# Optimization experiments

Hardware: AMD Instinct MI355X
Metric: run time of the kernel (lower is better)

## Reference

```python
import jax, jax.numpy as jnp
import numpy as np

B, T, F = 4096, 60, 64
H = 128          # num_hidden[0] == num_hidden[1]
FC1_IN, FC1_OUT = T * H, 512   # 7680 -> 512
LEN_OUT = 60


def setup_inputs() -> dict:
    key = jax.random.key(0)
    ks = jax.random.split(key, 14)
    s1 = 1.0 / np.sqrt(H)
    def u(k, shape, s):
        return jax.random.uniform(k, shape, jnp.float32, -s, s)
    return {
        "X_cont": jax.random.normal(ks[0], (B, T, F), jnp.float32),
        # LSTM layer 1 (PyTorch gate order i,f,g,o)
        "W_ih1": u(ks[1], (4 * H, F), s1),
        "W_hh1": u(ks[2], (4 * H, H), s1),
        "b_ih1": u(ks[3], (4 * H,), s1),
        "b_hh1": u(ks[4], (4 * H,), s1),
        # LSTM layer 2
        "W_ih2": u(ks[5], (4 * H, H), s1),
        "W_hh2": u(ks[6], (4 * H, H), s1),
        "b_ih2": u(ks[7], (4 * H,), s1),
        "b_hh2": u(ks[8], (4 * H,), s1),
        # FC head
        "W_fc1": u(ks[9], (FC1_OUT, FC1_IN), 1.0 / np.sqrt(FC1_IN)),
        "b_fc1": u(ks[10], (FC1_OUT,), 1.0 / np.sqrt(FC1_IN)),
        "W_fc2": u(ks[11], (LEN_OUT, FC1_OUT), 1.0 / np.sqrt(FC1_OUT)),
        "b_fc2": u(ks[12], (LEN_OUT,), 1.0 / np.sqrt(FC1_OUT)),
    }


def _lstm_layer(x, W_ih, W_hh, b_ih, b_hh):
    # x: [B,T,Fin]; zero initial (h,c); returns full hidden sequence [B,T,H]
    b, h = x.shape[0], W_hh.shape[1]
    # precompute input contribution for all timesteps (one big GEMM)
    xg = jnp.einsum('btf,gf->btg', x, W_ih) + b_ih + b_hh  # [B,T,4H]

    def step(carry, xt):
        hp, cp = carry
        g = xt + hp @ W_hh.T                                # [B,4H]
        i, f, gg, o = jnp.split(g, 4, axis=-1)
        i = jax.nn.sigmoid(i)
        f = jax.nn.sigmoid(f)
        gg = jnp.tanh(gg)
        o = jax.nn.sigmoid(o)
        c = f * cp + i * gg
        hn = o * jnp.tanh(c)
        return (hn, c), hn

    h0 = jnp.zeros((b, h), x.dtype)
    _, hs = jax.lax.scan(step, (h0, h0), jnp.swapaxes(xg, 0, 1))  # [T,B,H]
    return jnp.swapaxes(hs, 0, 1)


def reference(X_cont, W_ih1, W_hh1, b_ih1, b_hh1,
              W_ih2, W_hh2, b_ih2, b_hh2,
              W_fc1, b_fc1, W_fc2, b_fc2):
    b = X_cont.shape[0]
    h1 = _lstm_layer(X_cont, W_ih1, W_hh1, b_ih1, b_hh1)   # [B,T,H]
    h2 = _lstm_layer(h1, W_ih2, W_hh2, b_ih2, b_hh2)       # [B,T,H]
    flat = h2.reshape(b, -1)                               # [B, T*H] = [B,7680]
    fc1 = flat @ W_fc1.T + b_fc1                           # [B,512]
    fc2 = fc1 @ W_fc2.T + b_fc2                            # [B,length_out]
    return fc2.reshape(b, LEN_OUT, 1)
```

## Files before the change

kernel.cpp:

```cpp
#include <hip/hip_runtime.h>
#include <hip/hip_fp16.h>
#include <cstdint>

typedef _Float16 h16;
typedef _Float16 half8 __attribute__((ext_vector_type(8)));
typedef float floatx4 __attribute__((ext_vector_type(4)));

#define T_SZ 60
#define H_SZ 128
#define NB_FC1 7680
#define NKT   240

#define LOG2E  1.44269504088896340736f
#define LOG2E2 2.88539008177792681472f

__device__ __forceinline__ float sigm(float x) {
    float e = __builtin_amdgcn_exp2f(x * -LOG2E);
    return __builtin_amdgcn_rcpf(1.0f + e);
}
__device__ __forceinline__ float tanh_f(float x) {
    float e = __builtin_amdgcn_exp2f(x * LOG2E2);
    return 1.0f - 2.0f * __builtin_amdgcn_rcpf(e + 1.0f);
}

template<int INDIM, bool IN_F32, bool FUSE_FC>
__global__ __launch_bounds__(512, 1)
void lstm_layer(const void* __restrict__ in_v,
                const float* __restrict__ W_ih,
                const float* __restrict__ W_hh,
                const float* __restrict__ b_ih,
                const float* __restrict__ b_hh,
                h16* __restrict__ h_out,
                const h16* __restrict__ WcT,
                const float* __restrict__ bcv,
                float* __restrict__ out)
{
    constexpr int KT_IN = INDIM / 32;
    __shared__ __align__(16) h16 hist[16][16][H_SZ];

    const int tid  = threadIdx.x;
    const int w    = tid >> 6;
    const int lane = tid & 63;
    const int lrow = lane & 15;
    const int lgrp = lane >> 4;
    const size_t base_row = (size_t)blockIdx.x * 16;

    half8 wf_in[4][KT_IN];
    half8 wf_hh[4][4];
    float bias[4];

    #pragma unroll
    for (int q = 0; q < 4; ++q) {
        const int n = (w + 8 * q) * 16 + lrow;
        bias[q] = b_ih[n] + b_hh[n];
        #pragma unroll
        for (int kt = 0; kt < KT_IN; ++kt) {
            const float* p = W_ih + (size_t)n * INDIM + kt * 32 + lgrp * 8;
            half8 v;
            #pragma unroll
            for (int j = 0; j < 8; ++j) v[j] = (h16)p[j];
            wf_in[q][kt] = v;
        }
        #pragma unroll
        for (int kt = 0; kt < 4; ++kt) {
            const float* p = W_hh + (size_t)n * H_SZ + kt * 32 + lgrp * 8;
            half8 v;
            #pragma unroll
            for (int j = 0; j < 8; ++j) v[j] = (h16)p[j];
            wf_hh[q][kt] = v;
        }
    }

    const float* inF = (const float*)in_v;
    const h16*   inH = (const h16*)in_v;

    floatx4 raw[KT_IN][2];
    half8   xs[KT_IN];

    auto load_x = [&](int t) {
        #pragma unroll
        for (int kt = 0; kt < KT_IN; ++kt) {
            if constexpr (IN_F32) {
                const float* p = inF + ((base_row + lrow) * T_SZ + t) * INDIM + kt * 32 + lgrp * 8;
                raw[kt][0] = *(const floatx4*)(p);
                raw[kt][1] = *(const floatx4*)(p + 4);
            } else {
                xs[kt] = *(const half8*)(inH + ((base_row + lrow) * T_SZ + t) * INDIM + kt * 32 + lgrp * 8);
            }
        }
    };

    auto get_x = [&](half8 (&xf)[KT_IN]) {
        #pragma unroll
        for (int kt = 0; kt < KT_IN; ++kt) {
            if constexpr (IN_F32) {
                const auto p0 = __builtin_amdgcn_cvt_pkrtz(raw[kt][0][0], raw[kt][0][1]);
                const auto p1 = __builtin_amdgcn_cvt_pkrtz(raw[kt][0][2], raw[kt][0][3]);
                const auto p2 = __builtin_amdgcn_cvt_pkrtz(raw[kt][1][0], raw[kt][1][1]);
                const auto p3 = __builtin_amdgcn_cvt_pkrtz(raw[kt][1][2], raw[kt][1][3]);
                half8 v;
                v[0] = (h16)p0[0]; v[1] = (h16)p0[1]; v[2] = (h16)p1[0]; v[3] = (h16)p1[1];
                v[4] = (h16)p2[0]; v[5] = (h16)p2[1]; v[6] = (h16)p3[0]; v[7] = (h16)p3[1];
                xf[kt] = v;
            } else {
                xf[kt] = xs[kt];
            }
        }
    };

    floatx4 c4 = {0.f, 0.f, 0.f, 0.f};
    const int colW = 16 * w + lrow;

    auto flush = [&](int t) {
        half8 vals[4];
        int   time[4], row[4], cg[4];
        #pragma unroll
        for (int s = 0; s < 4; ++s) {
            const int u = tid + 512 * s;
            time[s] = t - 7 + (u >> 8);
            row[s]  = (u >> 4) & 15;
            cg[s]   = u & 15;
            vals[s] = *(const half8*)&hist[time[s] & 15][row[s]][(cg[s] * 8) ^ ((row[s] & 7) << 3)];
        }
        #pragma unroll
        for (int s = 0; s < 4; ++s)
            *(half8*)(h_out + ((base_row + row[s]) * T_SZ + time[s]) * H_SZ + cg[s] * 8) = vals[s];
    };

    floatx4 accA[4], accB[4];
    load_x(0);
    {
        half8 xf[KT_IN];
        get_x(xf);
        #pragma unroll
        for (int q = 0; q < 4; ++q) accA[q] = floatx4{bias[q], bias[q], bias[q], bias[q]};
        #pragma unroll
        for (int kt = 0; kt < KT_IN; ++kt)
            #pragma unroll
            for (int q = 0; q < 4; ++q)
                accA[q] = __builtin_amdgcn_mfma_f32_16x16x32_f16(xf[kt], wf_in[q][kt], accA[q], 0, 0, 0);
        load_x(1);
    }

    auto step = [&](int t, floatx4 (&accC)[4], floatx4 (&accN)[4]) {
        half8 hf[4];
        const bool have_h = (t > 0);
        if (have_h) {
            const h16* hb = &hist[(t - 1) & 15][0][0];
            #pragma unroll
            for (int kt = 0; kt < 4; ++kt) {
                const int col0 = kt * 32 + lgrp * 8;
                hf[kt] = *(const half8*)(hb + lrow * H_SZ + (col0 ^ ((lrow & 7) << 3)));
            }
        }

        if (t + 1 < T_SZ) {
            half8 xf[KT_IN];
            get_x(xf);
            #pragma unroll
            for (int q = 0; q < 4; ++q) accN[q] = floatx4{bias[q], bias[q], bias[q], bias[q]};
            #pragma unroll
            for (int kt = 0; kt < KT_IN; ++kt)
                #pragma unroll
                for (int q = 0; q < 4; ++q)
                    accN[q] = __builtin_amdgcn_mfma_f32_16x16x32_f16(xf[kt], wf_in[q][kt], accN[q], 0, 0, 0);
            if (t + 2 < T_SZ) load_x(t + 2);
        }

        if (have_h) {
            #pragma unroll
            for (int kt = 0; kt < 4; ++kt)
                #pragma unroll
                for (int q = 0; q < 4; ++q)
                    accC[q] = __builtin_amdgcn_mfma_f32_16x16x32_f16(hf[kt], wf_hh[q][kt], accC[q], 0, 0, 0);
        }

        h16 hcast[4];
        #pragma unroll
        for (int r = 0; r < 4; ++r) {
            const float gi = sigm(accC[0][r]);
            const float gf = sigm(accC[1][r]);
            const float gg = tanh_f(accC[2][r]);
            const float go = sigm(accC[3][r]);
            const float cc = gf * c4[r] + gi * gg;
            c4[r] = cc;
            hcast[r] = (h16)(go * tanh_f(cc));
        }
        h16* hb2 = &hist[t & 15][0][0];
        #pragma unroll
        for (int r = 0; r < 4; ++r) {
            const int rowW = lgrp * 4 + r;
            hb2[rowW * H_SZ + (colW ^ ((rowW & 7) << 3))] = hcast[r];
        }

        asm volatile("s_waitcnt lgkmcnt(0)" ::: "memory");
        __builtin_amdgcn_s_barrier();
        asm volatile("" ::: "memory");

        if (((t & 7) == 7) || (t == T_SZ - 1)) flush(t);
    };

    #pragma unroll 1
    for (int tt = 0; tt < T_SZ; tt += 2) {
        step(tt,     accA, accB);
        step(tt + 1, accB, accA);
    }

    if constexpr (FUSE_FC) {
        __syncthreads();

        floatx4 afc[4];
        #pragma unroll
        for (int q = 0; q < 4; ++q) afc[q] = floatx4{0.f, 0.f, 0.f, 0.f};

        const h16* arow = h_out + (base_row + lrow) * NB_FC1;

        auto ld = [&](int i, half8& a, half8 (&b)[4]) {
            const int ktg = w * 30 + i;
            const int k0  = ktg * 32 + lgrp * 8;
            a = *(const half8*)(arow + k0);
            #pragma unroll
            for (int q = 0; q < 4; ++q) {
                const int n = q * 16 + lrow;
                b[q] = 0;
                if (n < 60)
                    b[q] = *(const half8*)(WcT + ((size_t)ktg * 64 + n) * 32 + lgrp * 8);
            }
        };
        auto mm4 = [&](const half8& a, const half8 (&b)[4]) {
            #pragma unroll
            for (int q = 0; q < 4; ++q)
                afc[q] = __builtin_amdgcn_mfma_f32_16x16x32_f16(a, b[q], afc[q], 0, 0, 0);
        };

        half8 a0, a1, a2, b0[4], b1[4], b2[4];
        ld(0, a0, b0);
        ld(1, a1, b1);
        #pragma unroll 1
        for (int i = 0; i < 30; i += 3) {
            ld(i + 2, a2, b2);
            mm4(a0, b0);
            if (i + 3 < 30) ld(i + 3, a0, b0);
            mm4(a1, b1);
            if (i + 4 < 30) ld(i + 4, a1, b1);
            mm4(a2, b2);
        }

        float* red = (float*)&hist[0][0][0];
        #pragma unroll
        for (int q = 0; q < 4; ++q)
            #pragma unroll
            for (int r = 0; r < 4; ++r)
                red[(((w * 4 + q) * 16) + (lgrp * 4 + r)) * 16 + lrow] = afc[q][r];
        __syncthreads();

        #pragma unroll
        for (int s = 0; s < 2; ++s) {
            const int idx = tid + 512 * s;
            const int row = idx >> 6, col = idx & 63;
            if (col < 60) {
                const int q = col >> 4, cin = col & 15;
                float v = 0.f;
                #pragma unroll
                for (int ww = 0; ww < 8; ++ww)
                    v += red[(((ww * 4 + q) * 16) + row) * 16 + cin];
                out[(base_row + row) * 60 + col] = v + bcv[col];
            }
        }
    }
}

__global__ __launch_bounds__(256, 2)
void head_kernel(const float* __restrict__ W_fc1,
                 const float* __restrict__ W_fc2,
                 const float* __restrict__ b_fc1,
                 const float* __restrict__ b_fc2,
                 h16* __restrict__ WcT,
                 float* __restrict__ bc)
{
    const int tid  = threadIdx.x;
    if (blockIdx.x >= 120) {
        const int m = blockIdx.x - 120;
        const int t = tid;
        float p = W_fc2[m * 512 + t] * b_fc1[t] + W_fc2[m * 512 + 256 + t] * b_fc1[256 + t];
        #pragma unroll
        for (int off = 1; off < 64; off <<= 1) p += __shfl_xor(p, off);
        __shared__ float sred[4];
        if ((t & 63) == 0) sred[t >> 6] = p;
        __syncthreads();
        if (t == 0) bc[m] = sred[0] + sred[1] + sred[2] + sred[3] + b_fc2[m];
        return;
    }

    const int wv   = tid >> 6;
    const int lane = tid & 63;
    const int lrow = lane & 15;
    const int lgrp = lane >> 4;
    const int j0   = blockIdx.x * 64 + wv * 16;

    floatx4 acc[4];
    #pragma unroll
    for (int mt = 0; mt < 4; ++mt) acc[mt] = floatx4{0.f, 0.f, 0.f, 0.f};

    for (int kt = 0; kt < 16; ++kt) {
        const int k0 = kt * 32 + lgrp * 8;
        half8 bf;
        #pragma unroll
        for (int i = 0; i < 8; ++i)
            bf[i] = (h16)W_fc1[(size_t)(k0 + i) * NB_FC1 + j0 + lrow];
        #pragma unroll
        for (int mt = 0; mt < 4; ++mt) {
            const int m = mt * 16 + lrow;
            half8 af = {};
            if (m < 60) {
                const float* p = W_fc2 + (size_t)m * 512 + k0;
                const floatx4 f0 = *(const floatx4*)(p);
                const floatx4 f1 = *(const floatx4*)(p + 4);
                const auto p0 = __builtin_amdgcn_cvt_pkrtz(f0[0], f0[1]);
                const auto p1 = __builtin_amdgcn_cvt_pkrtz(f0[2], f0[3]);
                const auto p2 = __builtin_amdgcn_cvt_pkrtz(f1[0], f1[1]);
                const auto p3 = __builtin_amdgcn_cvt_pkrtz(f1[2], f1[3]);
                af[0] = (h16)p0[0]; af[1] = (h16)p0[1]; af[2] = (h16)p1[0]; af[3] = (h16)p1[1];
                af[4] = (h16)p2[0]; af[5] = (h16)p2[1]; af[6] = (h16)p3[0]; af[7] = (h16)p3[1];
            }
            acc[mt] = __builtin_amdgcn_mfma_f32_16x16x32_f16(af, bf, acc[mt], 0, 0, 0);
        }
    }

    #pragma unroll
    for (int mt = 0; mt < 4; ++mt)
        #pragma unroll
        for (int r = 0; r < 4; ++r) {
            const int m = mt * 16 + lgrp * 4 + r;
            const int j = j0 + lrow;
            if (m < 60)
                WcT[((size_t)(j >> 5) * 64 + m) * 32 + (j & 31)] = (h16)acc[mt][r];
        }
}

extern "C" void kernel_launch(void* const* d_in, const int* in_sizes, int n_in,
                              void* d_out, int out_size, void* d_ws, size_t ws_size,
                              hipStream_t stream)
{
    const float* X      = (const float*)d_in[0];
    const float* W_ih1  = (const float*)d_in[1];
    const float* W_hh1  = (const float*)d_in[2];
    const float* b_ih1  = (const float*)d_in[3];
    const float* b_hh1  = (const float*)d_in[4];
    const float* W_ih2  = (const float*)d_in[5];
    const float* W_hh2  = (const float*)d_in[6];
    const float* b_ih2  = (const float*)d_in[7];
    const float* b_hh2  = (const float*)d_in[8];
    const float* W_fc1  = (const float*)d_in[9];
    const float* b_fc1  = (const float*)d_in[10];
    const float* W_fc2  = (const float*)d_in[11];
    const float* b_fc2  = (const float*)d_in[12];

    h16* h1  = (h16*)d_ws;
    h16* h2  = h1 + (size_t)4096 * NB_FC1;
    h16* WcT = h2 + (size_t)4096 * NB_FC1;
    float* bc = (float*)(WcT + (size_t)NKT * 64 * 32);

    head_kernel<<<180, 256, 0, stream>>>(W_fc1, W_fc2, b_fc1, b_fc2, WcT, bc);
    lstm_layer<64,  true,  false><<<256, 512, 0, stream>>>(
        (const void*)X,  W_ih1, W_hh1, b_ih1, b_hh1, h1, nullptr, nullptr, nullptr);
    lstm_layer<128, false, true ><<<256, 512, 0, stream>>>(
        (const void*)h1, W_ih2, W_hh2, b_ih2, b_hh2, h2, WcT, bc, (float*)d_out);
}
```

Baseline: 213.0 us.

## Interleave two independent batch groups per block in layer-1 LSTM kernel

Adds a dedicated layer-1 LSTM kernel where each block processes two 16-row batch tiles, interleaving their input GEMMs, recurrent MFMAs and gate activations. The aim is to hide the serial recurrence latency (MFMA, LDS and transcendental dependencies) of one chain behind the other's work. The grid shrinks from 256 to 128 blocks, so fewer CUs are used. This trades parallelism across the device for instruction-level overlap within each block, and doubles the LDS history buffer.

```diff
diff --git a/kernel.cpp b/kernel.cpp
--- a/kernel.cpp
+++ b/kernel.cpp
@@ -21,6 +21,215 @@
 __device__ __forceinline__ float tanh_f(float x) {
     float e = __builtin_amdgcn_exp2f(x * LOG2E2);
     return 1.0f - 2.0f * __builtin_amdgcn_rcpf(e + 1.0f);
+}
+
+__global__ __launch_bounds__(512, 1)
+void lstm1_dual(const float* __restrict__ X,
+                const float* __restrict__ W_ih,
+                const float* __restrict__ W_hh,
+                const float* __restrict__ b_ih,
+                const float* __restrict__ b_hh,
+                h16* __restrict__ h_out)
+{
+    __shared__ __align__(16) h16 hist[2][16][16][H_SZ];
+
+    const int tid  = threadIdx.x;
+    const int w    = tid >> 6;
+    const int lane = tid & 63;
+    const int lrow = lane & 15;
+    const int lgrp = lane >> 4;
+    const size_t baseA = (size_t)blockIdx.x * 32;
+    const size_t baseB = baseA + 16;
+
+    half8 wf_in[4][2];
+    half8 wf_hh[4][4];
+    float bias[4];
+
+    #pragma unroll
+    for (int q = 0; q < 4; ++q) {
+        const int n = (w + 8 * q) * 16 + lrow;
+        bias[q] = b_ih[n] + b_hh[n];
+        #pragma unroll
+        for (int kt = 0; kt < 2; ++kt) {
+            const float* p = W_ih + (size_t)n * 64 + kt * 32 + lgrp * 8;
+            half8 v;
+            #pragma unroll
+            for (int j = 0; j < 8; ++j) v[j] = (h16)p[j];
+            wf_in[q][kt] = v;
+        }
+        #pragma unroll
+        for (int kt = 0; kt < 4; ++kt) {
+            const float* p = W_hh + (size_t)n * H_SZ + kt * 32 + lgrp * 8;
+            half8 v;
+            #pragma unroll
+            for (int j = 0; j < 8; ++j) v[j] = (h16)p[j];
+            wf_hh[q][kt] = v;
+        }
+    }
+
+    floatx4 rawA[2][2], rawB[2][2];
+
+    auto load_xA = [&](int t) {
+        #pragma unroll
+        for (int kt = 0; kt < 2; ++kt) {
+            const float* p = X + ((baseA + lrow) * T_SZ + t) * 64 + kt * 32 + lgrp * 8;
+            rawA[kt][0] = *(const floatx4*)(p);
+            rawA[kt][1] = *(const floatx4*)(p + 4);
+        }
+    };
+    auto load_xB = [&](int t) {
+        #pragma unroll
+        for (int kt = 0; kt < 2; ++kt) {
+            const float* p = X + ((baseB + lrow) * T_SZ + t) * 64 + kt * 32 + lgrp * 8;
+            rawB[kt][0] = *(const floatx4*)(p);
+            rawB[kt][1] = *(const floatx4*)(p + 4);
+        }
+    };
+    auto cvt = [&](const floatx4 (&raw)[2][2], half8 (&xf)[2]) {
+        #pragma unroll
+        for (int kt = 0; kt < 2; ++kt) {
+            const auto p0 = __builtin_amdgcn_cvt_pkrtz(raw[kt][0][0], raw[kt][0][1]);
+            const auto p1 = __builtin_amdgcn_cvt_pkrtz(raw[kt][0][2], raw[kt][0][3]);
+            const auto p2 = __builtin_amdgcn_cvt_pkrtz(raw[kt][1][0], raw[kt][1][1]);
+            const auto p3 = __builtin_amdgcn_cvt_pkrtz(raw[kt][1][2], raw[kt][1][3]);
+            half8 v;
+            v[0] = (h16)p0[0]; v[1] = (h16)p0[1]; v[2] = (h16)p1[0]; v[3] = (h16)p1[1];
+            v[4] = (h16)p2[0]; v[5] = (h16)p2[1]; v[6] = (h16)p3[0]; v[7] = (h16)p3[1];
+            xf[kt] = v;
+        }
+    };
+
+    floatx4 cA = {0.f, 0.f, 0.f, 0.f};
+    floatx4 cB = {0.f, 0.f, 0.f, 0.f};
+    const int colW = 16 * w + lrow;
+
+    auto flush = [&](int t) {
+        #pragma unroll
+        for (int g = 0; g < 2; ++g) {
+            const size_t base = g ? baseB : baseA;
+            half8 vals[4];
+            int   time[4], row[4], cg[4];
+            #pragma unroll
+            for (int s = 0; s < 4; ++s) {
+                const int u = tid + 512 * s;
+                time[s] = t - 7 + (u >> 8);
+                row[s]  = (u >> 4) & 15;
+                cg[s]   = u & 15;
+                vals[s] = *(const half8*)&hist[g][time[s] & 15][row[s]][(cg[s] * 8) ^ ((row[s] & 7) << 3)];
+            }
+            #pragma unroll
+            for (int s = 0; s < 4; ++s)
+                *(half8*)(h_out + ((base + row[s]) * T_SZ + time[s]) * H_SZ + cg[s] * 8) = vals[s];
+        }
+    };
+
+    load_xA(0);
+    load_xB(0);
+
+    #pragma unroll 1
+    for (int t = 0; t < T_SZ; ++t) {
+        const bool have_h = (t > 0);
+
+        half8 hfA[4];
+        if (have_h) {
+            const h16* hb = &hist[0][(t - 1) & 15][0][0];
+            #pragma unroll
+            for (int kt = 0; kt < 4; ++kt) {
+                const int col0 = kt * 32 + lgrp * 8;
+                hfA[kt] = *(const half8*)(hb + lrow * H_SZ + (col0 ^ ((lrow & 7) << 3)));
+            }
+        }
+
+        floatx4 accB4[4];
+        {
+            half8 xf[2];
+            cvt(rawB, xf);
+            #pragma unroll
+            for (int q = 0; q < 4; ++q) accB4[q] = floatx4{bias[q], bias[q], bias[q], bias[q]};
+            #pragma unroll
+            for (int kt = 0; kt < 2; ++kt)
+                #pragma unroll
+                for (int q = 0; q < 4; ++q)
+                    accB4[q] = __builtin_amdgcn_mfma_f32_16x16x32_f16(xf[kt], wf_in[q][kt], accB4[q], 0, 0, 0);
+            if (t + 1 < T_SZ) load_xB(t + 1);
+        }
+
+        floatx4 accA4[4];
+        {
+            half8 xf[2];
+            cvt(rawA, xf);
+            #pragma unroll
+            for (int q = 0; q < 4; ++q) accA4[q] = floatx4{bias[q], bias[q], bias[q], bias[q]};
+            #pragma unroll
+            for (int kt = 0; kt < 2; ++kt)
+                #pragma unroll
+                for (int q = 0; q < 4; ++q)
+                    accA4[q] = __builtin_amdgcn_mfma_f32_16x16x32_f16(xf[kt], wf_in[q][kt], accA4[q], 0, 0, 0);
+            if (t + 1 < T_SZ) load_xA(t + 1);
+        }
+        if (have_h) {
+            #pragma unroll
+            for (int kt = 0; kt < 4; ++kt)
+                #pragma unroll
+                for (int q = 0; q < 4; ++q)
+                    accA4[q] = __builtin_amdgcn_mfma_f32_16x16x32_f16(hfA[kt], wf_hh[q][kt], accA4[q], 0, 0, 0);
+        }
+
+        half8 hfB[4];
+        if (have_h) {
+            const h16* hb = &hist[1][(t - 1) & 15][0][0];
+            #pragma unroll
+            for (int kt = 0; kt < 4; ++kt) {
+                const int col0 = kt * 32 + lgrp * 8;
+                hfB[kt] = *(const half8*)(hb + lrow * H_SZ + (col0 ^ ((lrow & 7) << 3)));
+            }
+        }
+
+        {
+            h16* hb2 = &hist[0][t & 15][0][0];
+            #pragma unroll
+            for (int r = 0; r < 4; ++r) {
+                const float gi = sigm(accA4[0][r]);
+                const float gf = sigm(accA4[1][r]);
+                const float gg = tanh_f(accA4[2][r]);
+                const float go = sigm(accA4[3][r]);
+                const float cc = gf * cA[r] + gi * gg;
+                cA[r] = cc;
+                const h16 hh = (h16)(go * tanh_f(cc));
+                const int rowW = lgrp * 4 + r;
+                hb2[rowW * H_SZ + (colW ^ ((rowW & 7) << 3))] = hh;
+            }
+        }
+
+        if (have_h) {
+            #pragma unroll
+            for (int kt = 0; kt < 4; ++kt)
+                #pragma unroll
+                for (int q = 0; q < 4; ++q)
+                    accB4[q] = __builtin_amdgcn_mfma_f32_16x16x32_f16(hfB[kt], wf_hh[q][kt], accB4[q], 0, 0, 0);
+        }
+        {
+            h16* hb2 = &hist[1][t & 15][0][0];
+            #pragma unroll
+            for (int r = 0; r < 4; ++r) {
+                const float gi = sigm(accB4[0][r]);
+                const float gf = sigm(accB4[1][r]);
+                const float gg = tanh_f(accB4[2][r]);
+                const float go = sigm(accB4[3][r]);
+                const float cc = gf * cB[r] + gi * gg;
+                cB[r] = cc;
+                const h16 hh = (h16)(go * tanh_f(cc));
+                const int rowW = lgrp * 4 + r;
+                hb2[rowW * H_SZ + (colW ^ ((rowW & 7) << 3))] = hh;
+            }
+        }
+
+        asm volatile("s_waitcnt lgkmcnt(0)" ::: "memory");
+        __builtin_amdgcn_s_barrier();
+        asm volatile("" ::: "memory");
+
+        if (((t & 7) == 7) || (t == T_SZ - 1)) flush(t);
+    }
 }
 
 template<int INDIM, bool IN_F32, bool FUSE_FC>
@@ -362,8 +571,7 @@
     float* bc = (float*)(WcT + (size_t)NKT * 64 * 32);
 
     head_kernel<<<180, 256, 0, stream>>>(W_fc1, W_fc2, b_fc1, b_fc2, WcT, bc);
-    lstm_layer<64,  true,  false><<<256, 512, 0, stream>>>(
-        (const void*)X,  W_ih1, W_hh1, b_ih1, b_hh1, h1, nullptr, nullptr, nullptr);
+    lstm1_dual<<<128, 512, 0, stream>>>(X, W_ih1, W_hh1, b_ih1, b_hh1, h1);
     lstm_layer<128, false, true ><<<256, 512, 0, stream>>>(
         (const void*)h1, W_ih2, W_hh2, b_ih2, b_hh2, h2, WcT, bc, (float*)d_out);
 }
```

New measurement: 356.1 us, median of 3. +67.2%, slower.
